# Kernel optimization log

Measured on AMD Instinct MI355X. Metric: run time of the kernel, lower is better.

The kernel has to match this reference:

```python
import jax, jax.numpy as jnp
import numpy as np

N = 100000
E = 3200000
IN_DIM = 256
HIDDEN = 128


def spmm(rows, cols, vals, x, n):
    # y[r] = sum_e vals[e] * x[cols[e]] for edges with rows[e] == r
    return jax.ops.segment_sum(vals[:, None] * x[cols], rows, num_segments=n)


def setup_inputs() -> dict:
    key = jax.random.key(0)
    k = jax.random.split(key, 10)
    x = jax.random.normal(k[0], (N, IN_DIM), dtype=jnp.float32)
    edge_rows = jax.random.randint(k[1], (E,), 0, N, dtype=jnp.int32)
    edge_cols = jax.random.randint(k[2], (E,), 0, N, dtype=jnp.int32)
    edge_vals = jax.random.uniform(k[3], (E,), dtype=jnp.float32) / 32.0  # ~normalized adjacency
    s1 = 1.0 / np.sqrt(IN_DIM)
    s2 = 1.0 / np.sqrt(HIDDEN)
    w1 = jax.random.uniform(k[4], (IN_DIM, HIDDEN), minval=-s1, maxval=s1, dtype=jnp.float32)
    b1 = jax.random.uniform(k[5], (HIDDEN,), minval=-s1, maxval=s1, dtype=jnp.float32)
    w2 = jax.random.uniform(k[6], (HIDDEN, HIDDEN), minval=-s2, maxval=s2, dtype=jnp.float32)
    b2 = jax.random.uniform(k[7], (HIDDEN,), minval=-s2, maxval=s2, dtype=jnp.float32)
    wo = jax.random.uniform(k[8], (HIDDEN, 1), minval=-s2, maxval=s2, dtype=jnp.float32)
    bo = jax.random.uniform(k[9], (1,), minval=-s2, maxval=s2, dtype=jnp.float32)
    return {"x": x, "edge_rows": edge_rows, "edge_cols": edge_cols, "edge_vals": edge_vals,
            "w1": w1, "b1": b1, "w2": w2, "b2": b2, "wo": wo, "bo": bo}


def reference(x, edge_rows, edge_cols, edge_vals, w1, b1, w2, b2, wo, bo):
    n = x.shape[0]
    h1 = spmm(edge_rows, edge_cols, edge_vals, x, n)          # [N, in_dim]
    h1 = jax.nn.relu(h1 @ w1 + b1)                            # [N, hidden]
    h2 = spmm(edge_rows, edge_cols, edge_vals, h1, n)         # [N, hidden]
    h2 = jax.nn.relu(h2 @ w2 + b2)                            # [N, hidden]
    z = (h2 @ wo + bo).squeeze(-1)                            # [N]
    return z
```

## Files before the change

### kernel.cpp

```cpp
#include <hip/hip_runtime.h>
#include <hip/hip_bf16.h>


#define HID 128
#define CHUNK_E 16384

typedef __attribute__((ext_vector_type(8))) short bf16x8;
typedef __attribute__((ext_vector_type(4))) float f32x4;

__device__ __forceinline__ ushort f2bf(float f) {
    union { float f; unsigned u; } v; v.f = f;
    unsigned r = v.u + 0x7fffu + ((v.u >> 16) & 1u);
    return (ushort)(r >> 16);
}
__device__ __forceinline__ float bf2f(ushort u) {
    return __uint_as_float(((unsigned)u) << 16);
}

__global__ __launch_bounds__(256) void bhist_kernel(const int* __restrict__ rows,
                                                    int* __restrict__ histT,
                                                    int E, int nbucket, int nchunk) {
    __shared__ int h[512];
    const int t = threadIdx.x;
    const int c = blockIdx.x;
    for (int b = t; b < nbucket; b += 256) h[b] = 0;
    __syncthreads();
    const int estart = c * CHUNK_E;
    const int eend = min(estart + CHUNK_E, E);
    for (int e4 = estart + t * 4; e4 < eend; e4 += 1024) {
        if (e4 + 4 <= eend) {
            const int4 r4 = *reinterpret_cast<const int4*>(&rows[e4]);
            atomicAdd(&h[r4.x >> 9], 1);
            atomicAdd(&h[r4.y >> 9], 1);
            atomicAdd(&h[r4.z >> 9], 1);
            atomicAdd(&h[r4.w >> 9], 1);
        } else {
            for (int e = e4; e < eend; ++e) atomicAdd(&h[rows[e] >> 9], 1);
        }
    }
    __syncthreads();
    for (int b = t; b < nbucket; b += 256) histT[b * nchunk + c] = h[b];
}

__global__ __launch_bounds__(1024) void bscan_kernel(int* __restrict__ histT, int ntot,
                                                     int* __restrict__ rowptr, int n, int E) {
    __shared__ int s[1024];
    const int t = threadIdx.x;
    const int seq = (ntot + 1023) >> 10;
    const int i0 = t * seq;
    const int i1 = min(i0 + seq, ntot);
    int sum = 0;
    for (int i = i0; i < i1; ++i) sum += histT[i];
    s[t] = sum;
    __syncthreads();
    for (int off = 1; off < 1024; off <<= 1) {
        int u = (t >= off) ? s[t - off] : 0;
        __syncthreads();
        s[t] += u;
        __syncthreads();
    }
    int run = s[t] - sum;
    for (int i = i0; i < i1; ++i) {
        int v = histT[i];
        histT[i] = run;
        run += v;
    }
    if (t == 0) rowptr[n] = E;
}

__global__ __launch_bounds__(256) void partition_kernel(const int* __restrict__ rows,
                                                        const int* __restrict__ cols,
                                                        const float* __restrict__ vals,
                                                        const int* __restrict__ baseT,
                                                        int2* __restrict__ bcv,
                                                        int E, int nbucket, int nchunk) {
    __shared__ int cur[512];
    const int t = threadIdx.x;
    const int c = blockIdx.x;
    for (int b = t; b < nbucket; b += 256) cur[b] = baseT[b * nchunk + c];
    __syncthreads();
    const int estart = c * CHUNK_E;
    const int eend = min(estart + CHUNK_E, E);
    for (int e4 = estart + t * 4; e4 < eend; e4 += 1024) {
        if (e4 + 4 <= eend) {
            const int4 r4 = *reinterpret_cast<const int4*>(&rows[e4]);
            const int4 c4 = *reinterpret_cast<const int4*>(&cols[e4]);
            const float4 v4 = *reinterpret_cast<const float4*>(&vals[e4]);
            int p;
            p = atomicAdd(&cur[r4.x >> 9], 1);
            bcv[p] = make_int2(c4.x | ((r4.x & 511) << 17), __float_as_int(v4.x));
            p = atomicAdd(&cur[r4.y >> 9], 1);
            bcv[p] = make_int2(c4.y | ((r4.y & 511) << 17), __float_as_int(v4.y));
            p = atomicAdd(&cur[r4.z >> 9], 1);
            bcv[p] = make_int2(c4.z | ((r4.z & 511) << 17), __float_as_int(v4.z));
            p = atomicAdd(&cur[r4.w >> 9], 1);
            bcv[p] = make_int2(c4.w | ((r4.w & 511) << 17), __float_as_int(v4.w));
        } else {
            for (int e = e4; e < eend; ++e) {
                int r = rows[e];
                int p = atomicAdd(&cur[r >> 9], 1);
                bcv[p] = make_int2(cols[e] | ((r & 511) << 17), __float_as_int(vals[e]));
            }
        }
    }
}

__global__ __launch_bounds__(256) void finalize_kernel(const int2* __restrict__ bcv,
                                                       const int* __restrict__ baseT,
                                                       int* __restrict__ rowptr,
                                                       int2* __restrict__ epair,
                                                       int N, int E, int nchunk, int nbucket) {
    __shared__ int cnt[512];
    __shared__ int part[256];
    const int t = threadIdx.x;
    const int b = blockIdx.x;
    const int rowbase = b << 9;
    const int nrows_b = min(512, N - rowbase);
    const int bstart = baseT[b * nchunk];
    const int bend = (b + 1 < nbucket) ? baseT[(b + 1) * nchunk] : E;
    cnt[t] = 0;
    cnt[t + 256] = 0;
    __syncthreads();
    for (int e = bstart + t; e < bend; e += 256) {
        const int w0 = reinterpret_cast<const int*>(bcv)[2 * e];
        atomicAdd(&cnt[w0 >> 17], 1);
    }
    __syncthreads();
    const int a0 = cnt[2 * t];
    const int a1 = cnt[2 * t + 1];
    part[t] = a0 + a1;
    __syncthreads();
    for (int off = 1; off < 256; off <<= 1) {
        int u = (t >= off) ? part[t - off] : 0;
        __syncthreads();
        part[t] += u;
        __syncthreads();
    }
    const int excl = part[t] - (a0 + a1);
    cnt[2 * t] = bstart + excl;
    cnt[2 * t + 1] = bstart + excl + a0;
    if (2 * t < nrows_b) rowptr[rowbase + 2 * t] = bstart + excl;
    if (2 * t + 1 < nrows_b) rowptr[rowbase + 2 * t + 1] = bstart + excl + a0;
    __syncthreads();
    for (int e = bstart + t; e < bend; e += 256) {
        const int2 w = bcv[e];
        const int p = atomicAdd(&cnt[w.x >> 17], 1);
        epair[p] = make_int2(w.x & 0x1FFFF, w.y);
    }
}

template <int K, bool ABF16>
__global__ __launch_bounds__(256) void mfma_gemm(const void* __restrict__ Aptr,
                                                 const float* __restrict__ W,
                                                 ushort* __restrict__ C, int nrows) {
    __shared__ __align__(16) ushort wt[128 * K];
    const int t = threadIdx.x;
    for (int idx = t; idx < K * 32; idx += 256) {
        const int c4 = (idx & 31) << 2;
        const int k = idx >> 5;
        const float4 w4 = *reinterpret_cast<const float4*>(&W[k * 128 + c4]);
        const float wf[4] = {w4.x, w4.y, w4.z, w4.w};
        #pragma unroll
        for (int j = 0; j < 4; ++j) {
            const int c = c4 + j;
            const unsigned byteoff = (unsigned)(((c * K + k) * 2) ^ ((c & 7) << 4));
            *reinterpret_cast<ushort*>(reinterpret_cast<char*>(wt) + byteoff) = f2bf(wf[j]);
        }
    }
    __syncthreads();

    const int lane = t & 63;
    const int wv = t >> 6;
    const int r = lane & 15;
    const int g = lane >> 4;
    const int row_base = blockIdx.x * 128 + wv * 32;
    const unsigned xorv = (unsigned)((r & 7) << 4);
    f32x4 acc[2][8] = {};

    for (int s = 0; s < K / 32; ++s) {
        const int kb = s * 32 + g * 8;
        bf16x8 a[2];
        #pragma unroll
        for (int f = 0; f < 2; ++f) {
            int row = row_base + f * 16 + r;
            if (row >= nrows) row = nrows - 1;
            if (ABF16) {
                a[f] = *reinterpret_cast<const bf16x8*>(
                    (const ushort*)Aptr + (size_t)row * K + kb);
            } else {
                const float* Af = (const float*)Aptr + (size_t)row * K + kb;
                const float4 v0 = *reinterpret_cast<const float4*>(Af);
                const float4 v1 = *reinterpret_cast<const float4*>(Af + 4);
                bf16x8 av;
                av[0] = (short)f2bf(v0.x); av[1] = (short)f2bf(v0.y);
                av[2] = (short)f2bf(v0.z); av[3] = (short)f2bf(v0.w);
                av[4] = (short)f2bf(v1.x); av[5] = (short)f2bf(v1.y);
                av[6] = (short)f2bf(v1.z); av[7] = (short)f2bf(v1.w);
                a[f] = av;
            }
        }
        #pragma unroll
        for (int c = 0; c < 8; ++c) {
            const unsigned boff = ((unsigned)(((c * 16 + r) * K + kb) * 2)) ^ xorv;
            const bf16x8 b = *reinterpret_cast<const bf16x8*>(
                reinterpret_cast<char*>(wt) + boff);
            acc[0][c] = __builtin_amdgcn_mfma_f32_16x16x32_bf16(a[0], b, acc[0][c], 0, 0, 0);
            acc[1][c] = __builtin_amdgcn_mfma_f32_16x16x32_bf16(a[1], b, acc[1][c], 0, 0, 0);
        }
    }
    #pragma unroll
    for (int f = 0; f < 2; ++f) {
        #pragma unroll
        for (int j = 0; j < 4; ++j) {
            const int row = row_base + f * 16 + g * 4 + j;
            if (row < nrows) {
                #pragma unroll
                for (int c = 0; c < 8; ++c) {
                    C[(size_t)row * HID + c * 16 + r] = f2bf(acc[f][c][j]);
                }
            }
        }
    }
}

template <bool FINAL>
__global__ __launch_bounds__(256) void spmm_kernel(const int* __restrict__ row_ptr,
                                                   const int2* __restrict__ epair,
                                                   const ushort* __restrict__ X,
                                                   const float* __restrict__ bias,
                                                   const float* __restrict__ wo,
                                                   const float* __restrict__ bo,
                                                   void* __restrict__ out, int nrows) {
    const int wave = threadIdx.x >> 6;
    const int lane = threadIdx.x & 63;
    const int row = blockIdx.x * 4 + wave;
    if (row >= nrows) return;
    const int e0 = row_ptr[row];
    const int e1 = row_ptr[row + 1];
    float ax = 0.f, ay = 0.f;
    int e = e0;
    for (; e + 8 <= e1; e += 8) {
        int2 ev[8];
        #pragma unroll
        for (int i = 0; i < 8; ++i) ev[i] = epair[e + i];
        unsigned xv[8];
        #pragma unroll
        for (int i = 0; i < 8; ++i)
            xv[i] = *reinterpret_cast<const unsigned*>(&X[(size_t)ev[i].x * HID + lane * 2]);
        #pragma unroll
        for (int i = 0; i < 8; ++i) {
            const float v = __int_as_float(ev[i].y);
            ax += v * bf2f((ushort)(xv[i] & 0xffffu));
            ay += v * bf2f((ushort)(xv[i] >> 16));
        }
    }
    for (; e < e1; ++e) {
        const int2 evt = epair[e];
        const unsigned xu = *reinterpret_cast<const unsigned*>(&X[(size_t)evt.x * HID + lane * 2]);
        const float v = __int_as_float(evt.y);
        ax += v * bf2f((ushort)(xu & 0xffffu));
        ay += v * bf2f((ushort)(xu >> 16));
    }
    const float hx = fmaxf(ax + bias[lane * 2], 0.f);
    const float hy = fmaxf(ay + bias[lane * 2 + 1], 0.f);
    if (!FINAL) {
        const unsigned packed = (unsigned)f2bf(hx) | ((unsigned)f2bf(hy) << 16);
        reinterpret_cast<unsigned*>(out)[(size_t)row * (HID / 2) + lane] = packed;
    } else {
        float p = hx * wo[lane * 2] + hy * wo[lane * 2 + 1];
        #pragma unroll
        for (int off = 32; off > 0; off >>= 1) p += __shfl_down(p, off, 64);
        if (lane == 0) reinterpret_cast<float*>(out)[row] = p + bo[0];
    }
}

extern "C" void kernel_launch(void* const* d_in, const int* in_sizes, int n_in,
                              void* d_out, int out_size, void* d_ws, size_t ws_size,
                              hipStream_t stream) {
    const float* x        = (const float*)d_in[0];
    const int*   e_rows   = (const int*)d_in[1];
    const int*   e_cols   = (const int*)d_in[2];
    const float* e_vals   = (const float*)d_in[3];
    const float* w1       = (const float*)d_in[4];
    const float* b1       = (const float*)d_in[5];
    const float* w2       = (const float*)d_in[6];
    const float* b2       = (const float*)d_in[7];
    const float* wo       = (const float*)d_in[8];
    const float* bo       = (const float*)d_in[9];
    float* z = (float*)d_out;

    const int IN_DIM = 256;
    const int N = in_sizes[0] / IN_DIM;
    const int E = in_sizes[1];
    const int NCHUNK = (E + CHUNK_E - 1) / CHUNK_E;
    const int NBUCKET = (N + 511) >> 9;

    size_t off = 0;
    auto alloc = [&](size_t bytes) {
        void* p = (char*)d_ws + off;
        off += (bytes + 255) & ~(size_t)255;
        return p;
    };
    ushort* bufA  = (ushort*)alloc((size_t)N * HID * 2);
    ushort* bufB  = (ushort*)alloc((size_t)N * HID * 2);
    int*   rowptr = (int*)alloc((size_t)(N + 1) * 4);
    int*   histT  = (int*)alloc((size_t)NBUCKET * NCHUNK * 4);
    int2*  epair  = (int2*)alloc((size_t)E * 8);
    int2*  bcv    = (int2*)alloc((size_t)E * 8);
    (void)ws_size;

    bhist_kernel<<<NCHUNK, 256, 0, stream>>>(e_rows, histT, E, NBUCKET, NCHUNK);
    bscan_kernel<<<1, 1024, 0, stream>>>(histT, NBUCKET * NCHUNK, rowptr, N, E);
    partition_kernel<<<NCHUNK, 256, 0, stream>>>(e_rows, e_cols, e_vals, histT, bcv, E, NBUCKET, NCHUNK);
    finalize_kernel<<<NBUCKET, 256, 0, stream>>>(bcv, histT, rowptr, epair, N, E, NCHUNK, NBUCKET);

    const int gemm_grid = (N + 127) / 128;
    mfma_gemm<256, false><<<gemm_grid, 256, 0, stream>>>(x, w1, bufA, N);
    spmm_kernel<false><<<(N + 3) / 4, 256, 0, stream>>>(rowptr, epair, bufA, b1, nullptr, nullptr, bufB, N);

    mfma_gemm<128, true><<<gemm_grid, 256, 0, stream>>>(bufB, w2, bufA, N);
    spmm_kernel<true><<<(N + 3) / 4, 256, 0, stream>>>(rowptr, epair, bufA, b2, wo, bo, z, N);
}
```

Measured before the change: 632.7 us.

## Parallelize bucket scan, tile GEMM weights by K, and widen SpMM unroll

Replaces the single-block sequential scan over the bucket histogram with a three-kernel reduce, scan and emit scheme that spreads the work across many blocks. The GEMM now loads weights into shared memory in 128-deep K slices, so the K=256 layer uses half the LDS, which may allow more blocks per CU at the cost of an extra barrier. The SpMM gather loop is unrolled to 16 edges to keep more loads in flight, at the cost of more registers and longer scalar tail loops. The scan change adds two extra kernel launches.

Measured after the change: 638.3 us. About the same (+0.9%).

```diff
diff --git a/kernel.cpp b/kernel.cpp
--- a/kernel.cpp
+++ b/kernel.cpp
@@ -42,16 +42,28 @@
     for (int b = t; b < nbucket; b += 256) histT[b * nchunk + c] = h[b];
 }
 
-__global__ __launch_bounds__(1024) void bscan_kernel(int* __restrict__ histT, int ntot,
+__global__ __launch_bounds__(256) void bsum_kernel(const int* __restrict__ histT,
+                                                   int* __restrict__ bsums, int ntot) {
+    __shared__ int part[256];
+    const int t = threadIdx.x;
+    const int i0 = blockIdx.x * 512 + 2 * t;
+    int a = (i0 < ntot) ? histT[i0] : 0;
+    int b = (i0 + 1 < ntot) ? histT[i0 + 1] : 0;
+    part[t] = a + b;
+    __syncthreads();
+    for (int off = 128; off > 0; off >>= 1) {
+        if (t < off) part[t] += part[t + off];
+        __syncthreads();
+    }
+    if (t == 0) bsums[blockIdx.x] = part[0];
+}
+
+__global__ __launch_bounds__(1024) void bscan_kernel(int* __restrict__ bsums, int nseg,
                                                      int* __restrict__ rowptr, int n, int E) {
     __shared__ int s[1024];
     const int t = threadIdx.x;
-    const int seq = (ntot + 1023) >> 10;
-    const int i0 = t * seq;
-    const int i1 = min(i0 + seq, ntot);
-    int sum = 0;
-    for (int i = i0; i < i1; ++i) sum += histT[i];
-    s[t] = sum;
+    int v = (t < nseg) ? bsums[t] : 0;
+    s[t] = v;
     __syncthreads();
     for (int off = 1; off < 1024; off <<= 1) {
         int u = (t >= off) ? s[t - off] : 0;
@@ -59,13 +71,28 @@
         s[t] += u;
         __syncthreads();
     }
-    int run = s[t] - sum;
-    for (int i = i0; i < i1; ++i) {
-        int v = histT[i];
-        histT[i] = run;
-        run += v;
-    }
+    if (t < nseg) bsums[t] = s[t] - v;
     if (t == 0) rowptr[n] = E;
+}
+
+__global__ __launch_bounds__(256) void bemit_kernel(int* __restrict__ histT,
+                                                    const int* __restrict__ bsums, int ntot) {
+    __shared__ int part[256];
+    const int t = threadIdx.x;
+    const int i0 = blockIdx.x * 512 + 2 * t;
+    const int a = (i0 < ntot) ? histT[i0] : 0;
+    const int b = (i0 + 1 < ntot) ? histT[i0 + 1] : 0;
+    part[t] = a + b;
+    __syncthreads();
+    for (int off = 1; off < 256; off <<= 1) {
+        int u = (t >= off) ? part[t - off] : 0;
+        __syncthreads();
+        part[t] += u;
+        __syncthreads();
+    }
+    const int base = bsums[blockIdx.x] + part[t] - (a + b);
+    if (i0 < ntot) histT[i0] = base;
+    if (i0 + 1 < ntot) histT[i0 + 1] = base + a;
 }
 
 __global__ __launch_bounds__(256) void partition_kernel(const int* __restrict__ rows,
@@ -153,22 +180,9 @@
 __global__ __launch_bounds__(256) void mfma_gemm(const void* __restrict__ Aptr,
                                                  const float* __restrict__ W,
                                                  ushort* __restrict__ C, int nrows) {
-    __shared__ __align__(16) ushort wt[128 * K];
-    const int t = threadIdx.x;
-    for (int idx = t; idx < K * 32; idx += 256) {
-        const int c4 = (idx & 31) << 2;
-        const int k = idx >> 5;
-        const float4 w4 = *reinterpret_cast<const float4*>(&W[k * 128 + c4]);
-        const float wf[4] = {w4.x, w4.y, w4.z, w4.w};
-        #pragma unroll
-        for (int j = 0; j < 4; ++j) {
-            const int c = c4 + j;
-            const unsigned byteoff = (unsigned)(((c * K + k) * 2) ^ ((c & 7) << 4));
-            *reinterpret_cast<ushort*>(reinterpret_cast<char*>(wt) + byteoff) = f2bf(wf[j]);
-        }
-    }
-    __syncthreads();
-
+    constexpr int KH = 128;
+    __shared__ __align__(16) ushort wt[128 * KH];
+    const int t = threadIdx.x;
     const int lane = t & 63;
     const int wv = t >> 6;
     const int r = lane & 15;
@@ -177,35 +191,53 @@
     const unsigned xorv = (unsigned)((r & 7) << 4);
     f32x4 acc[2][8] = {};
 
-    for (int s = 0; s < K / 32; ++s) {
-        const int kb = s * 32 + g * 8;
-        bf16x8 a[2];
-        #pragma unroll
-        for (int f = 0; f < 2; ++f) {
-            int row = row_base + f * 16 + r;
-            if (row >= nrows) row = nrows - 1;
-            if (ABF16) {
-                a[f] = *reinterpret_cast<const bf16x8*>(
-                    (const ushort*)Aptr + (size_t)row * K + kb);
-            } else {
-                const float* Af = (const float*)Aptr + (size_t)row * K + kb;
-                const float4 v0 = *reinterpret_cast<const float4*>(Af);
-                const float4 v1 = *reinterpret_cast<const float4*>(Af + 4);
-                bf16x8 av;
-                av[0] = (short)f2bf(v0.x); av[1] = (short)f2bf(v0.y);
-                av[2] = (short)f2bf(v0.z); av[3] = (short)f2bf(v0.w);
-                av[4] = (short)f2bf(v1.x); av[5] = (short)f2bf(v1.y);
-                av[6] = (short)f2bf(v1.z); av[7] = (short)f2bf(v1.w);
-                a[f] = av;
-            }
-        }
-        #pragma unroll
-        for (int c = 0; c < 8; ++c) {
-            const unsigned boff = ((unsigned)(((c * 16 + r) * K + kb) * 2)) ^ xorv;
-            const bf16x8 b = *reinterpret_cast<const bf16x8*>(
-                reinterpret_cast<char*>(wt) + boff);
-            acc[0][c] = __builtin_amdgcn_mfma_f32_16x16x32_bf16(a[0], b, acc[0][c], 0, 0, 0);
-            acc[1][c] = __builtin_amdgcn_mfma_f32_16x16x32_bf16(a[1], b, acc[1][c], 0, 0, 0);
+    for (int kh = 0; kh < K; kh += KH) {
+        if (kh) __syncthreads();
+        for (int idx = t; idx < KH * 32; idx += 256) {
+            const int c4 = (idx & 31) << 2;
+            const int k = idx >> 5;
+            const float4 w4 = *reinterpret_cast<const float4*>(&W[(kh + k) * 128 + c4]);
+            const float wf[4] = {w4.x, w4.y, w4.z, w4.w};
+            #pragma unroll
+            for (int j = 0; j < 4; ++j) {
+                const int c = c4 + j;
+                const unsigned byteoff = (unsigned)(((c * KH + k) * 2) ^ ((c & 7) << 4));
+                *reinterpret_cast<ushort*>(reinterpret_cast<char*>(wt) + byteoff) = f2bf(wf[j]);
+            }
+        }
+        __syncthreads();
+
+        for (int s = 0; s < KH / 32; ++s) {
+            const int kbg = kh + s * 32 + g * 8;
+            const int kbl = s * 32 + g * 8;
+            bf16x8 a[2];
+            #pragma unroll
+            for (int f = 0; f < 2; ++f) {
+                int row = row_base + f * 16 + r;
+                if (row >= nrows) row = nrows - 1;
+                if (ABF16) {
+                    a[f] = *reinterpret_cast<const bf16x8*>(
+                        (const ushort*)Aptr + (size_t)row * K + kbg);
+                } else {
+                    const float* Af = (const float*)Aptr + (size_t)row * K + kbg;
+                    const float4 v0 = *reinterpret_cast<const float4*>(Af);
+                    const float4 v1 = *reinterpret_cast<const float4*>(Af + 4);
+                    bf16x8 av;
+                    av[0] = (short)f2bf(v0.x); av[1] = (short)f2bf(v0.y);
+                    av[2] = (short)f2bf(v0.z); av[3] = (short)f2bf(v0.w);
+                    av[4] = (short)f2bf(v1.x); av[5] = (short)f2bf(v1.y);
+                    av[6] = (short)f2bf(v1.z); av[7] = (short)f2bf(v1.w);
+                    a[f] = av;
+                }
+            }
+            #pragma unroll
+            for (int c = 0; c < 8; ++c) {
+                const unsigned boff = ((unsigned)(((c * 16 + r) * KH + kbl) * 2)) ^ xorv;
+                const bf16x8 b = *reinterpret_cast<const bf16x8*>(
+                    reinterpret_cast<char*>(wt) + boff);
+                acc[0][c] = __builtin_amdgcn_mfma_f32_16x16x32_bf16(a[0], b, acc[0][c], 0, 0, 0);
+                acc[1][c] = __builtin_amdgcn_mfma_f32_16x16x32_bf16(a[1], b, acc[1][c], 0, 0, 0);
+            }
         }
     }
     #pragma unroll
@@ -239,16 +271,16 @@
     const int e1 = row_ptr[row + 1];
     float ax = 0.f, ay = 0.f;
     int e = e0;
-    for (; e + 8 <= e1; e += 8) {
-        int2 ev[8];
-        #pragma unroll
-        for (int i = 0; i < 8; ++i) ev[i] = epair[e + i];
-        unsigned xv[8];
-        #pragma unroll
-        for (int i = 0; i < 8; ++i)
+    for (; e + 16 <= e1; e += 16) {
+        int2 ev[16];
+        #pragma unroll
+        for (int i = 0; i < 16; ++i) ev[i] = epair[e + i];
+        unsigned xv[16];
+        #pragma unroll
+        for (int i = 0; i < 16; ++i)
             xv[i] = *reinterpret_cast<const unsigned*>(&X[(size_t)ev[i].x * HID + lane * 2]);
         #pragma unroll
-        for (int i = 0; i < 8; ++i) {
+        for (int i = 0; i < 16; ++i) {
             const float v = __int_as_float(ev[i].y);
             ax += v * bf2f((ushort)(xv[i] & 0xffffu));
             ay += v * bf2f((ushort)(xv[i] >> 16));
@@ -294,6 +326,8 @@
     const int E = in_sizes[1];
     const int NCHUNK = (E + CHUNK_E - 1) / CHUNK_E;
     const int NBUCKET = (N + 511) >> 9;
+    const int NTOT = NBUCKET * NCHUNK;
+    const int NSEG = (NTOT + 511) / 512;
 
     size_t off = 0;
     auto alloc = [&](size_t bytes) {
@@ -304,13 +338,16 @@
     ushort* bufA  = (ushort*)alloc((size_t)N * HID * 2);
     ushort* bufB  = (ushort*)alloc((size_t)N * HID * 2);
     int*   rowptr = (int*)alloc((size_t)(N + 1) * 4);
-    int*   histT  = (int*)alloc((size_t)NBUCKET * NCHUNK * 4);
+    int*   histT  = (int*)alloc((size_t)NTOT * 4);
+    int*   bsums  = (int*)alloc((size_t)NSEG * 4);
     int2*  epair  = (int2*)alloc((size_t)E * 8);
     int2*  bcv    = (int2*)alloc((size_t)E * 8);
     (void)ws_size;
 
     bhist_kernel<<<NCHUNK, 256, 0, stream>>>(e_rows, histT, E, NBUCKET, NCHUNK);
-    bscan_kernel<<<1, 1024, 0, stream>>>(histT, NBUCKET * NCHUNK, rowptr, N, E);
+    bsum_kernel<<<NSEG, 256, 0, stream>>>(histT, bsums, NTOT);
+    bscan_kernel<<<1, 1024, 0, stream>>>(bsums, NSEG, rowptr, N, E);
+    bemit_kernel<<<NSEG, 256, 0, stream>>>(histT, bsums, NTOT);
     partition_kernel<<<NCHUNK, 256, 0, stream>>>(e_rows, e_cols, e_vals, histT, bcv, E, NBUCKET, NCHUNK);
     finalize_kernel<<<NBUCKET, 256, 0, stream>>>(bcv, histT, rowptr, epair, N, E, NCHUNK, NBUCKET);
 
```
